# Kernel optimization log

Hardware: AMD Instinct MI355X
Metric: run time of the kernel (lower is better)

The kernel has to match this reference:

```python
import jax, jax.numpy as jnp
import numpy as np

B, S, D, H = 2, 2048, 1024, 16
HD = D // H  # head dim = 64


def setup_inputs() -> dict:
    key = jax.random.key(0)
    ks = jax.random.split(key, 8)
    s = 0.02
    return {
        "Q": jax.random.normal(ks[0], (B, S, D), jnp.float32),
        "K": jax.random.normal(ks[1], (B, S, D), jnp.float32),
        "V": jax.random.normal(ks[2], (B, S, D), jnp.float32),
        "mask": jax.random.randint(ks[3], (1, 1, S, S), 0, 2, jnp.int32),
        "Wq": jax.random.normal(ks[4], (D, D), jnp.float32) * s,
        "bq": jnp.zeros((D,), jnp.float32),
        "Wk": jax.random.normal(ks[5], (D, D), jnp.float32) * s,
        "bk": jnp.zeros((D,), jnp.float32),
        "Wv": jax.random.normal(ks[6], (D, D), jnp.float32) * s,
        "bv": jnp.zeros((D,), jnp.float32),
        "Wo": jax.random.normal(ks[7], (D, D), jnp.float32) * s,
        "bo": jnp.zeros((D,), jnp.float32),
    }


def reference(Q, K, V, mask, Wq, bq, Wk, bk, Wv, bv, Wo, bo):
    b = Q.shape[0]
    # QKV projections, split into heads: [B,S,D] -> [B,H,S,HD]
    q = (Q @ Wq + bq).reshape(b, -1, H, HD).transpose(0, 2, 1, 3)
    k = (K @ Wk + bk).reshape(b, -1, H, HD).transpose(0, 2, 1, 3)
    v = (V @ Wv + bv).reshape(b, -1, H, HD).transpose(0, 2, 1, 3)
    # scaled dot-product attention with full [B,H,S,S] scores (as in source)
    scale = jnp.sqrt(jnp.asarray(HD, q.dtype))
    scores = jnp.einsum("bhqd,bhkd->bhqk", q, k) / scale
    scores = jnp.where(mask == 0, -jnp.inf, scores)
    attn = jax.nn.softmax(scores, axis=-1)
    ctx = jnp.einsum("bhqk,bhkd->bhqd", attn, v)
    # merge heads and output projection
    concat = ctx.transpose(0, 2, 1, 3).reshape(b, -1, H * HD)
    return concat @ Wo + bo
```

## Files before the change

### kernel.cpp

```cpp
#include <hip/hip_runtime.h>


using s8v = __attribute__((ext_vector_type(8))) short;
using f4v = __attribute__((ext_vector_type(4))) float;
typedef unsigned long long u64;

__device__ __forceinline__ unsigned short f2bf(float f) {
  union { float f; unsigned int u; } v; v.f = f;
  return (unsigned short)((v.u + 0x7fffu + ((v.u >> 16) & 1u)) >> 16);
}

__device__ __forceinline__ void gll16(const void* g, void* l) {
  __builtin_amdgcn_global_load_lds(
      (const __attribute__((address_space(1))) unsigned int*)g,
      (__attribute__((address_space(3))) unsigned int*)l, 16, 0, 0);
}

__global__ void prep_kernel(const float* __restrict__ Q, const float* __restrict__ K,
                            const float* __restrict__ V,
                            unsigned short* __restrict__ qb, unsigned short* __restrict__ kb,
                            unsigned short* __restrict__ vb,
                            const float* __restrict__ W0, const float* __restrict__ W1,
                            const float* __restrict__ W2, const float* __restrict__ W3,
                            unsigned short* __restrict__ T0, unsigned short* __restrict__ T1,
                            unsigned short* __restrict__ T2, unsigned short* __restrict__ T3,
                            const int* __restrict__ mask, u64* __restrict__ bm) {
  __shared__ unsigned short t[64][72];
  const int bid = blockIdx.x, tid = threadIdx.x;
  if (bid < 12288) {
    int z = bid >> 12;
    int idx = (bid & 4095) * 256 + tid;
    const float* in = (z == 0) ? Q : (z == 1) ? K : V;
    unsigned short* out = (z == 0) ? qb : (z == 1) ? kb : vb;
    float4 v = ((const float4*)in)[idx];
    ushort4 o;
    o.x = f2bf(v.x); o.y = f2bf(v.y); o.z = f2bf(v.z); o.w = f2bf(v.w);
    ((ushort4*)out)[idx] = o;
  } else if (bid < 13312) {
    int b = bid - 12288;
    int z = b >> 8, rem = b & 255;
    int k0 = (rem >> 4) * 64, n0 = (rem & 15) * 64;
    const float* W = (z == 0) ? W0 : (z == 1) ? W1 : (z == 2) ? W2 : W3;
    unsigned short* Wt = (z == 0) ? T0 : (z == 1) ? T1 : (z == 2) ? T2 : T3;
    for (int p = 0; p < 4; ++p) {
      int idx = p * 256 + tid;
      int row = idx >> 4, c4 = idx & 15;
      float4 v = *(const float4*)&W[(size_t)(k0 + row) * 1024 + n0 + c4 * 4];
      t[row][c4 * 4 + 0] = f2bf(v.x);
      t[row][c4 * 4 + 1] = f2bf(v.y);
      t[row][c4 * 4 + 2] = f2bf(v.z);
      t[row][c4 * 4 + 3] = f2bf(v.w);
    }
    __syncthreads();
    for (int p = 0; p < 2; ++p) {
      int idx = p * 256 + tid;
      int j = idx >> 3, c8 = idx & 7;
      unsigned short tmp[8];
      for (int i = 0; i < 8; ++i) tmp[i] = t[c8 * 8 + i][j];
      uint4 o;
      o.x = tmp[0] | ((unsigned)tmp[1] << 16);
      o.y = tmp[2] | ((unsigned)tmp[3] << 16);
      o.z = tmp[4] | ((unsigned)tmp[5] << 16);
      o.w = tmp[6] | ((unsigned)tmp[7] << 16);
      *(uint4*)&Wt[(size_t)(n0 + j) * 1024 + k0 + c8 * 8] = o;
    }
  } else {
    int b = bid - 13312;
    int gw = (b * 256 + tid) >> 6;
    int lane = tid & 63;
    int mv = mask[(size_t)gw * 64 + lane];
    u64 bal = __ballot(mv != 0);
    if (lane == 0) bm[gw] = bal;
  }
}

__global__ __launch_bounds__(256) void proj3_kernel(
    const unsigned short* __restrict__ A0, const unsigned short* __restrict__ A1,
    const unsigned short* __restrict__ A2,
    const unsigned short* __restrict__ W0, const unsigned short* __restrict__ W1,
    const unsigned short* __restrict__ W2,
    const float* __restrict__ b0, const float* __restrict__ b1, const float* __restrict__ b2,
    unsigned short* __restrict__ oq, unsigned short* __restrict__ ok,
    unsigned short* __restrict__ ovt) {
  const int z = blockIdx.z;
  const unsigned short* A  = (z == 0) ? A0 : (z == 1) ? A1 : A2;
  const unsigned short* Wt = (z == 0) ? W0 : (z == 1) ? W1 : W2;
  const float* bias        = (z == 0) ? b0 : (z == 1) ? b1 : b2;

  __shared__ __align__(16) unsigned short As[64 * 32];
  __shared__ __align__(16) unsigned short Bs[128 * 32];

  const int tid = threadIdx.x;
  const int lane = tid & 63, w = tid >> 6, ln = lane & 15, quad = lane >> 4;
  const int wm = (w & 1) * 32, wn = (w >> 1) * 64;
  const int m0 = blockIdx.x * 64, n0 = blockIdx.y * 128;

  const int slr = lane >> 2;
  const int schunk = (lane & 3) ^ ((lane >> 3) & 3);
  const int cfrag = (quad ^ ((ln >> 1) & 3)) * 8;

  f4v zero = {0.f, 0.f, 0.f, 0.f};
  f4v acc[2][4];
  for (int mi = 0; mi < 2; ++mi)
    for (int ni = 0; ni < 4; ++ni) acc[mi][ni] = zero;

  for (int kt = 0; kt < 1024; kt += 32) {
    __syncthreads();
    gll16(&A[(size_t)(m0 + w * 16 + slr) * 1024 + kt + schunk * 8],        &As[(w * 16) * 32]);
    gll16(&Wt[(size_t)(n0 + w * 32 + slr) * 1024 + kt + schunk * 8],       &Bs[(w * 32) * 32]);
    gll16(&Wt[(size_t)(n0 + w * 32 + 16 + slr) * 1024 + kt + schunk * 8],  &Bs[(w * 32 + 16) * 32]);
    __syncthreads();
    s8v a[2], b[4];
    for (int mi = 0; mi < 2; ++mi) a[mi] = *(const s8v*)&As[(wm + mi * 16 + ln) * 32 + cfrag];
    for (int ni = 0; ni < 4; ++ni) b[ni] = *(const s8v*)&Bs[(wn + ni * 16 + ln) * 32 + cfrag];
    if (z < 2) {
      for (int mi = 0; mi < 2; ++mi)
        for (int ni = 0; ni < 4; ++ni)
          acc[mi][ni] = __builtin_amdgcn_mfma_f32_16x16x32_bf16(a[mi], b[ni], acc[mi][ni], 0, 0, 0);
    } else {
      for (int mi = 0; mi < 2; ++mi)
        for (int ni = 0; ni < 4; ++ni)
          acc[mi][ni] = __builtin_amdgcn_mfma_f32_16x16x32_bf16(b[ni], a[mi], acc[mi][ni], 0, 0, 0);
    }
  }

  if (z < 2) {
    const float qscale = (z == 0) ? 0.18033688f : 1.0f;
    unsigned short* outp = (z == 0) ? oq : ok;
    for (int mi = 0; mi < 2; ++mi) {
      int rb = m0 + wm + mi * 16 + quad * 4;
      int b_ = rb >> 11;
      for (int ni = 0; ni < 4; ++ni) {
        int col = n0 + wn + ni * 16 + ln;
        float bvv = bias[col];
        int h = col >> 6, hd = col & 63;
        size_t ob = (size_t)(b_ * 16 + h) * 2048;
        for (int r = 0; r < 4; ++r) {
          int s = (rb + r) & 2047;
          outp[(ob + s) * 64 + hd] = f2bf((acc[mi][ni][r] + bvv) * qscale);
        }
      }
    }
  } else {
    for (int ni = 0; ni < 4; ++ni) {
      for (int r = 0; r < 4; ++r) {
        int colw = n0 + wn + ni * 16 + quad * 4 + r;
        int h = colw >> 6, hd = colw & 63;
        float bvv = bias[colw];
        for (int mi = 0; mi < 2; ++mi) {
          int sg = m0 + wm + mi * 16 + ln;
          int b_ = sg >> 11, ss = sg & 2047;
          ovt[((size_t)(b_ * 16 + h) * 64 + hd) * 2048 + ss] = f2bf(acc[mi][ni][r] + bvv);
        }
      }
    }
  }
}

__global__ __launch_bounds__(512) void flash_kernel(
    const unsigned short* __restrict__ q, const unsigned short* __restrict__ k,
    const unsigned short* __restrict__ vt, const u64* __restrict__ bm,
    unsigned short* __restrict__ ctx) {
  __shared__ __align__(16) unsigned short qp_s[128][72];
  __shared__ __align__(16) unsigned short k_s[64][72];
  __shared__ __align__(16) unsigned short v_s[80][72];

  const int tid = threadIdx.x;
  const int lane = tid & 63, w = tid >> 6, ln = lane & 15, quad = lane >> 4;
  const int q0 = blockIdx.x * 128;
  const int bh = blockIdx.y;
  const unsigned short* qg  = q  + ((size_t)bh * 2048 + q0) * 64;
  const unsigned short* kgb = k  + (size_t)bh * 2048 * 64;
  const unsigned short* vgb = vt + (size_t)bh * 64 * 2048;

  for (int j = 0; j < 3; ++j) {
    int idx = j * 512 + tid;
    if (idx < 16 * 72) ((unsigned short*)v_s[64])[idx] = 0;
  }
  for (int p = 0; p < 2; ++p) {
    int c = p * 512 + tid;
    int row = c >> 3, c8 = c & 7;
    *(uint4*)&qp_s[row][c8 * 8] = *(const uint4*)&qg[(size_t)row * 64 + c8 * 8];
  }
  __syncthreads();
  if (tid < 64) v_s[64][tid] = 0x3F80;
  __syncthreads();

  s8v aq0 = *(const s8v*)&qp_s[w * 16 + ln][quad * 8];
  s8v aq1 = *(const s8v*)&qp_s[w * 16 + ln][32 + quad * 8];
  s8v bones0 = *(const s8v*)&v_s[64 + ln][quad * 8];
  s8v bones1 = *(const s8v*)&v_s[64 + ln][32 + quad * 8];

  const int srow = tid >> 3, sc8 = tid & 7;

  const u64* bmr = bm + (size_t)(q0 + w * 16 + ln) * 32;

  uint4 kr = *(const uint4*)&kgb[(size_t)srow * 64 + sc8 * 8];
  uint4 vr = *(const uint4*)&vgb[(size_t)srow * 2048 + sc8 * 8];
  u64 mwc = bmr[0], mwn;

  f4v zero = {0.f, 0.f, 0.f, 0.f};
  f4v l_acc = zero;
  f4v o_acc[4];
  for (int ni = 0; ni < 4; ++ni) o_acc[ni] = zero;

  for (int kt = 0; kt < 2048; kt += 64) {
    *(uint4*)&k_s[srow][sc8 * 8] = kr;
    *(uint4*)&v_s[srow][sc8 * 8] = vr;
    if (kt + 64 < 2048) {
      int ktn = kt + 64;
      kr = *(const uint4*)&kgb[(size_t)(ktn + srow) * 64 + sc8 * 8];
      vr = *(const uint4*)&vgb[(size_t)srow * 2048 + ktn + sc8 * 8];
      mwn = bmr[ktn >> 6];
    }
    __syncthreads();

    f4v sc[4];
    for (int ni = 0; ni < 4; ++ni) {
      s8v ak0 = *(const s8v*)&k_s[ni * 16 + ln][quad * 8];
      s8v ak1 = *(const s8v*)&k_s[ni * 16 + ln][32 + quad * 8];
      f4v t = zero;
      t = __builtin_amdgcn_mfma_f32_16x16x32_bf16(ak0, aq0, t, 0, 0, 0);
      t = __builtin_amdgcn_mfma_f32_16x16x32_bf16(ak1, aq1, t, 0, 0, 0);
      sc[ni] = t;
    }

    {
      u64 m = mwc >> (quad * 4);
      unsigned mlo = (unsigned)m, mhi = (unsigned)(m >> 32);
      for (int ni = 0; ni < 4; ++ni) {
        unsigned msel = ((ni < 2) ? mlo : mhi) >> ((ni & 1) * 16);
        unsigned u0 = __float_as_uint(__builtin_amdgcn_exp2f(sc[ni][0]) * (float)(msel & 1u));
        unsigned u1 = __float_as_uint(__builtin_amdgcn_exp2f(sc[ni][1]) * (float)((msel >> 1) & 1u));
        unsigned u2 = __float_as_uint(__builtin_amdgcn_exp2f(sc[ni][2]) * (float)((msel >> 2) & 1u));
        unsigned u3 = __float_as_uint(__builtin_amdgcn_exp2f(sc[ni][3]) * (float)((msel >> 3) & 1u));
        unsigned plo = __builtin_amdgcn_perm(u1, u0, 0x07060302);
        unsigned phi = __builtin_amdgcn_perm(u3, u2, 0x07060302);
        *(u64*)&qp_s[w * 16 + ln][ni * 16 + quad * 4] = plo | ((u64)phi << 32);
      }
      mwc = mwn;
    }

    s8v ap0 = *(const s8v*)&qp_s[w * 16 + ln][quad * 8];
    s8v ap1 = *(const s8v*)&qp_s[w * 16 + ln][32 + quad * 8];
    for (int ni = 0; ni < 4; ++ni) {
      s8v bv0 = *(const s8v*)&v_s[ni * 16 + ln][quad * 8];
      s8v bv1 = *(const s8v*)&v_s[ni * 16 + ln][32 + quad * 8];
      o_acc[ni] = __builtin_amdgcn_mfma_f32_16x16x32_bf16(ap0, bv0, o_acc[ni], 0, 0, 0);
      o_acc[ni] = __builtin_amdgcn_mfma_f32_16x16x32_bf16(ap1, bv1, o_acc[ni], 0, 0, 0);
    }
    l_acc = __builtin_amdgcn_mfma_f32_16x16x32_bf16(ap0, bones0, l_acc, 0, 0, 0);
    l_acc = __builtin_amdgcn_mfma_f32_16x16x32_bf16(ap1, bones1, l_acc, 0, 0, 0);
    __syncthreads();
  }

  int b_ = bh >> 4, h = bh & 15;
  for (int r = 0; r < 4; ++r) {
    float lr = __shfl(l_acc[r], quad * 16);
    float inv = 1.f / lr;
    int srow_ = q0 + w * 16 + quad * 4 + r;
    size_t base = ((size_t)b_ * 2048 + srow_) * 1024 + h * 64;
    for (int ni = 0; ni < 4; ++ni)
      ctx[base + ni * 16 + ln] = f2bf(o_acc[ni][r] * inv);
  }
}

__global__ __launch_bounds__(256) void gemm_out_kernel(
    const unsigned short* __restrict__ A, const unsigned short* __restrict__ Wt,
    const float* __restrict__ bias, float* __restrict__ out) {
  __shared__ __align__(16) unsigned short As[64 * 32];
  __shared__ __align__(16) unsigned short Bs[128 * 32];

  const int tid = threadIdx.x;
  const int lane = tid & 63, w = tid >> 6, ln = lane & 15, quad = lane >> 4;
  const int wm = (w & 1) * 32, wn = (w >> 1) * 64;
  const int m0 = blockIdx.x * 64, n0 = blockIdx.y * 128;

  const int slr = lane >> 2;
  const int schunk = (lane & 3) ^ ((lane >> 3) & 3);
  const int cfrag = (quad ^ ((ln >> 1) & 3)) * 8;

  f4v zero = {0.f, 0.f, 0.f, 0.f};
  f4v acc[2][4];
  for (int mi = 0; mi < 2; ++mi)
    for (int ni = 0; ni < 4; ++ni) acc[mi][ni] = zero;

  for (int kt = 0; kt < 1024; kt += 32) {
    __syncthreads();
    gll16(&A[(size_t)(m0 + w * 16 + slr) * 1024 + kt + schunk * 8],        &As[(w * 16) * 32]);
    gll16(&Wt[(size_t)(n0 + w * 32 + slr) * 1024 + kt + schunk * 8],       &Bs[(w * 32) * 32]);
    gll16(&Wt[(size_t)(n0 + w * 32 + 16 + slr) * 1024 + kt + schunk * 8],  &Bs[(w * 32 + 16) * 32]);
    __syncthreads();
    s8v a[2], b[4];
    for (int mi = 0; mi < 2; ++mi) a[mi] = *(const s8v*)&As[(wm + mi * 16 + ln) * 32 + cfrag];
    for (int ni = 0; ni < 4; ++ni) b[ni] = *(const s8v*)&Bs[(wn + ni * 16 + ln) * 32 + cfrag];
    for (int mi = 0; mi < 2; ++mi)
      for (int ni = 0; ni < 4; ++ni)
        acc[mi][ni] = __builtin_amdgcn_mfma_f32_16x16x32_bf16(a[mi], b[ni], acc[mi][ni], 0, 0, 0);
  }

  for (int mi = 0; mi < 2; ++mi) {
    int rb = m0 + wm + mi * 16 + quad * 4;
    for (int ni = 0; ni < 4; ++ni) {
      int col = n0 + wn + ni * 16 + ln;
      float bvv = bias[col];
      for (int r = 0; r < 4; ++r)
        out[(size_t)(rb + r) * 1024 + col] = acc[mi][ni][r] + bvv;
    }
  }
}

extern "C" void kernel_launch(void* const* d_in, const int* in_sizes, int n_in,
                              void* d_out, int out_size, void* d_ws, size_t ws_size,
                              hipStream_t stream) {
  const float* Q  = (const float*)d_in[0];
  const float* K  = (const float*)d_in[1];
  const float* V  = (const float*)d_in[2];
  const int* mask = (const int*)d_in[3];
  const float* Wq = (const float*)d_in[4];
  const float* bq = (const float*)d_in[5];
  const float* Wk = (const float*)d_in[6];
  const float* bk = (const float*)d_in[7];
  const float* Wv = (const float*)d_in[8];
  const float* bv = (const float*)d_in[9];
  const float* Wo = (const float*)d_in[10];
  const float* bo = (const float*)d_in[11];
  float* out = (float*)d_out;

  char* ws = (char*)d_ws;
  const size_t MB = 1u << 20;
  unsigned short* qb  = (unsigned short*)(ws + 0 * MB);
  unsigned short* kb  = (unsigned short*)(ws + 8 * MB);
  unsigned short* vb  = (unsigned short*)(ws + 16 * MB);
  unsigned short* wqt = (unsigned short*)(ws + 24 * MB);
  unsigned short* wkt = (unsigned short*)(ws + 26 * MB);
  unsigned short* wvt = (unsigned short*)(ws + 28 * MB);
  unsigned short* wot = (unsigned short*)(ws + 30 * MB);
  unsigned short* qh  = (unsigned short*)(ws + 32 * MB);
  unsigned short* kh  = (unsigned short*)(ws + 40 * MB);
  unsigned short* vth = (unsigned short*)(ws + 48 * MB);
  u64* bm             = (u64*)(ws + 56 * MB);
  unsigned short* ctx = (unsigned short*)(ws + 16 * MB);

  prep_kernel<<<29696, 256, 0, stream>>>(Q, K, V, qb, kb, vb,
                                         Wq, Wk, Wv, Wo, wqt, wkt, wvt, wot,
                                         mask, bm);
  proj3_kernel<<<dim3(64, 8, 3), 256, 0, stream>>>(qb, kb, vb, wqt, wkt, wvt,
                                                   bq, bk, bv, qh, kh, vth);
  flash_kernel<<<dim3(16, 32), 512, 0, stream>>>(qh, kh, vth, bm, ctx);
  gemm_out_kernel<<<dim3(64, 8), 256, 0, stream>>>(ctx, wot, bo, out);
}
```

Measured before the change: 258.0 us.

## Rework flash attention on 32x32 MFMA with register-resident P and double-buffered K/V

The attention kernel drops from 8 waves of 16 query rows to 4 waves of 32 rows and uses 32x32x16 bf16 MFMAs. The P tile is repacked into A-operand layout in registers with v_permlane32_swap instead of being written to and read back from LDS. K/V tiles are double-buffered in LDS so the next tile is staged during compute, leaving one barrier per iteration. Each wave now holds more accumulators, so register pressure rises and occupancy may fall.

```diff
diff --git a/kernel.cpp b/kernel.cpp
--- a/kernel.cpp
+++ b/kernel.cpp
@@ -3,11 +3,16 @@
 
 using s8v = __attribute__((ext_vector_type(8))) short;
 using f4v = __attribute__((ext_vector_type(4))) float;
+using f16v = __attribute__((ext_vector_type(16))) float;
 typedef unsigned long long u64;
 
 __device__ __forceinline__ unsigned short f2bf(float f) {
   union { float f; unsigned int u; } v; v.f = f;
   return (unsigned short)((v.u + 0x7fffu + ((v.u >> 16) & 1u)) >> 16);
+}
+
+__device__ __forceinline__ unsigned pkbf(float lo, float hi2) {
+  return __builtin_amdgcn_perm(__float_as_uint(hi2), __float_as_uint(lo), 0x07060302);
 }
 
 __device__ __forceinline__ void gll16(const void* g, void* l) {
@@ -157,111 +162,137 @@
   }
 }
 
-__global__ __launch_bounds__(512) void flash_kernel(
+__global__ __launch_bounds__(256) void flash_kernel(
     const unsigned short* __restrict__ q, const unsigned short* __restrict__ k,
     const unsigned short* __restrict__ vt, const u64* __restrict__ bm,
     unsigned short* __restrict__ ctx) {
-  __shared__ __align__(16) unsigned short qp_s[128][72];
-  __shared__ __align__(16) unsigned short k_s[64][72];
-  __shared__ __align__(16) unsigned short v_s[80][72];
+  __shared__ __align__(16) unsigned short k_s[2][64][72];
+  __shared__ __align__(16) unsigned short v_s[2][64][72];
 
   const int tid = threadIdx.x;
-  const int lane = tid & 63, w = tid >> 6, ln = lane & 15, quad = lane >> 4;
+  const int lane = tid & 63, w = tid >> 6;
+  const int l31 = lane & 31, hi = lane >> 5;
   const int q0 = blockIdx.x * 128;
   const int bh = blockIdx.y;
   const unsigned short* qg  = q  + ((size_t)bh * 2048 + q0) * 64;
   const unsigned short* kgb = k  + (size_t)bh * 2048 * 64;
   const unsigned short* vgb = vt + (size_t)bh * 64 * 2048;
 
-  for (int j = 0; j < 3; ++j) {
-    int idx = j * 512 + tid;
-    if (idx < 16 * 72) ((unsigned short*)v_s[64])[idx] = 0;
-  }
-  for (int p = 0; p < 2; ++p) {
-    int c = p * 512 + tid;
-    int row = c >> 3, c8 = c & 7;
-    *(uint4*)&qp_s[row][c8 * 8] = *(const uint4*)&qg[(size_t)row * 64 + c8 * 8];
-  }
+  const int qrow = w * 32 + l31;
+  s8v qf[4];
+#pragma unroll
+  for (int c = 0; c < 4; ++c)
+    qf[c] = *(const s8v*)&qg[(size_t)qrow * 64 + c * 16 + hi * 8];
+
+  const u64* bmr = bm + (size_t)(q0 + qrow) * 32;
+
+  s8v ones;
+#pragma unroll
+  for (int i = 0; i < 8; ++i) ones[i] = (short)0x3F80;
+
+  const int srow = tid >> 3, sc8 = tid & 7;
+
+  uint4 kr0 = *(const uint4*)&kgb[(size_t)srow * 64 + sc8 * 8];
+  uint4 kr1 = *(const uint4*)&kgb[(size_t)(srow + 32) * 64 + sc8 * 8];
+  uint4 vr0 = *(const uint4*)&vgb[(size_t)srow * 2048 + sc8 * 8];
+  uint4 vr1 = *(const uint4*)&vgb[(size_t)(srow + 32) * 2048 + sc8 * 8];
+  *(uint4*)&k_s[0][srow][sc8 * 8] = kr0;
+  *(uint4*)&k_s[0][srow + 32][sc8 * 8] = kr1;
+  *(uint4*)&v_s[0][srow][sc8 * 8] = vr0;
+  *(uint4*)&v_s[0][srow + 32][sc8 * 8] = vr1;
+  kr0 = *(const uint4*)&kgb[(size_t)(64 + srow) * 64 + sc8 * 8];
+  kr1 = *(const uint4*)&kgb[(size_t)(64 + srow + 32) * 64 + sc8 * 8];
+  vr0 = *(const uint4*)&vgb[(size_t)srow * 2048 + 64 + sc8 * 8];
+  vr1 = *(const uint4*)&vgb[(size_t)(srow + 32) * 2048 + 64 + sc8 * 8];
   __syncthreads();
-  if (tid < 64) v_s[64][tid] = 0x3F80;
-  __syncthreads();
-
-  s8v aq0 = *(const s8v*)&qp_s[w * 16 + ln][quad * 8];
-  s8v aq1 = *(const s8v*)&qp_s[w * 16 + ln][32 + quad * 8];
-  s8v bones0 = *(const s8v*)&v_s[64 + ln][quad * 8];
-  s8v bones1 = *(const s8v*)&v_s[64 + ln][32 + quad * 8];
-
-  const int srow = tid >> 3, sc8 = tid & 7;
-
-  const u64* bmr = bm + (size_t)(q0 + w * 16 + ln) * 32;
-
-  uint4 kr = *(const uint4*)&kgb[(size_t)srow * 64 + sc8 * 8];
-  uint4 vr = *(const uint4*)&vgb[(size_t)srow * 2048 + sc8 * 8];
-  u64 mwc = bmr[0], mwn;
-
-  f4v zero = {0.f, 0.f, 0.f, 0.f};
-  f4v l_acc = zero;
-  f4v o_acc[4];
-  for (int ni = 0; ni < 4; ++ni) o_acc[ni] = zero;
+
+  f16v o0, o1, lac;
+#pragma unroll
+  for (int i = 0; i < 16; ++i) { o0[i] = 0.f; o1[i] = 0.f; lac[i] = 0.f; }
 
   for (int kt = 0; kt < 2048; kt += 64) {
-    *(uint4*)&k_s[srow][sc8 * 8] = kr;
-    *(uint4*)&v_s[srow][sc8 * 8] = vr;
+    const int cur = (kt >> 6) & 1;
+    u64 mwc = bmr[kt >> 6];
+
     if (kt + 64 < 2048) {
-      int ktn = kt + 64;
-      kr = *(const uint4*)&kgb[(size_t)(ktn + srow) * 64 + sc8 * 8];
-      vr = *(const uint4*)&vgb[(size_t)srow * 2048 + ktn + sc8 * 8];
-      mwn = bmr[ktn >> 6];
-    }
-    __syncthreads();
-
-    f4v sc[4];
-    for (int ni = 0; ni < 4; ++ni) {
-      s8v ak0 = *(const s8v*)&k_s[ni * 16 + ln][quad * 8];
-      s8v ak1 = *(const s8v*)&k_s[ni * 16 + ln][32 + quad * 8];
-      f4v t = zero;
-      t = __builtin_amdgcn_mfma_f32_16x16x32_bf16(ak0, aq0, t, 0, 0, 0);
-      t = __builtin_amdgcn_mfma_f32_16x16x32_bf16(ak1, aq1, t, 0, 0, 0);
-      sc[ni] = t;
-    }
-
-    {
-      u64 m = mwc >> (quad * 4);
-      unsigned mlo = (unsigned)m, mhi = (unsigned)(m >> 32);
-      for (int ni = 0; ni < 4; ++ni) {
-        unsigned msel = ((ni < 2) ? mlo : mhi) >> ((ni & 1) * 16);
-        unsigned u0 = __float_as_uint(__builtin_amdgcn_exp2f(sc[ni][0]) * (float)(msel & 1u));
-        unsigned u1 = __float_as_uint(__builtin_amdgcn_exp2f(sc[ni][1]) * (float)((msel >> 1) & 1u));
-        unsigned u2 = __float_as_uint(__builtin_amdgcn_exp2f(sc[ni][2]) * (float)((msel >> 2) & 1u));
-        unsigned u3 = __float_as_uint(__builtin_amdgcn_exp2f(sc[ni][3]) * (float)((msel >> 3) & 1u));
-        unsigned plo = __builtin_amdgcn_perm(u1, u0, 0x07060302);
-        unsigned phi = __builtin_amdgcn_perm(u3, u2, 0x07060302);
-        *(u64*)&qp_s[w * 16 + ln][ni * 16 + quad * 4] = plo | ((u64)phi << 32);
-      }
-      mwc = mwn;
-    }
-
-    s8v ap0 = *(const s8v*)&qp_s[w * 16 + ln][quad * 8];
-    s8v ap1 = *(const s8v*)&qp_s[w * 16 + ln][32 + quad * 8];
-    for (int ni = 0; ni < 4; ++ni) {
-      s8v bv0 = *(const s8v*)&v_s[ni * 16 + ln][quad * 8];
-      s8v bv1 = *(const s8v*)&v_s[ni * 16 + ln][32 + quad * 8];
-      o_acc[ni] = __builtin_amdgcn_mfma_f32_16x16x32_bf16(ap0, bv0, o_acc[ni], 0, 0, 0);
-      o_acc[ni] = __builtin_amdgcn_mfma_f32_16x16x32_bf16(ap1, bv1, o_acc[ni], 0, 0, 0);
-    }
-    l_acc = __builtin_amdgcn_mfma_f32_16x16x32_bf16(ap0, bones0, l_acc, 0, 0, 0);
-    l_acc = __builtin_amdgcn_mfma_f32_16x16x32_bf16(ap1, bones1, l_acc, 0, 0, 0);
-    __syncthreads();
-  }
-
-  int b_ = bh >> 4, h = bh & 15;
-  for (int r = 0; r < 4; ++r) {
-    float lr = __shfl(l_acc[r], quad * 16);
-    float inv = 1.f / lr;
-    int srow_ = q0 + w * 16 + quad * 4 + r;
-    size_t base = ((size_t)b_ * 2048 + srow_) * 1024 + h * 64;
-    for (int ni = 0; ni < 4; ++ni)
-      ctx[base + ni * 16 + ln] = f2bf(o_acc[ni][r] * inv);
+      const int nxt = cur ^ 1;
+      *(uint4*)&k_s[nxt][srow][sc8 * 8] = kr0;
+      *(uint4*)&k_s[nxt][srow + 32][sc8 * 8] = kr1;
+      *(uint4*)&v_s[nxt][srow][sc8 * 8] = vr0;
+      *(uint4*)&v_s[nxt][srow + 32][sc8 * 8] = vr1;
+      if (kt + 128 < 2048) {
+        const int kn = kt + 128;
+        kr0 = *(const uint4*)&kgb[(size_t)(kn + srow) * 64 + sc8 * 8];
+        kr1 = *(const uint4*)&kgb[(size_t)(kn + srow + 32) * 64 + sc8 * 8];
+        vr0 = *(const uint4*)&vgb[(size_t)srow * 2048 + kn + sc8 * 8];
+        vr1 = *(const uint4*)&vgb[(size_t)(srow + 32) * 2048 + kn + sc8 * 8];
+      }
+    }
+
+    f16v s0, s1;
+#pragma unroll
+    for (int i = 0; i < 16; ++i) { s0[i] = 0.f; s1[i] = 0.f; }
+#pragma unroll
+    for (int c = 0; c < 4; ++c) {
+      s8v ak0 = *(const s8v*)&k_s[cur][l31][c * 16 + hi * 8];
+      s8v ak1 = *(const s8v*)&k_s[cur][32 + l31][c * 16 + hi * 8];
+      s0 = __builtin_amdgcn_mfma_f32_32x32x16_bf16(ak0, qf[c], s0, 0, 0, 0);
+      s1 = __builtin_amdgcn_mfma_f32_32x32x16_bf16(ak1, qf[c], s1, 0, 0, 0);
+    }
+
+    const u64 mq = mwc >> (4 * hi);
+    s8v pf[4];
+#pragma unroll
+    for (int ni = 0; ni < 2; ++ni) {
+      const unsigned half = (unsigned)(mq >> (32 * ni));
+      float p[16];
+#pragma unroll
+      for (int g = 0; g < 4; ++g) {
+        const unsigned nib = (half >> (8 * g)) & 0xFu;
+#pragma unroll
+        for (int m = 0; m < 4; ++m) {
+          const float sv = (ni ? s1[g * 4 + m] : s0[g * 4 + m]);
+          p[g * 4 + m] = __builtin_amdgcn_exp2f(sv) * (float)((nib >> m) & 1u);
+        }
+      }
+#pragma unroll
+      for (int kcl = 0; kcl < 2; ++kcl) {
+        const int rb = 8 * kcl;
+        unsigned x0 = pkbf(p[rb + 0], p[rb + 1]);
+        unsigned x1 = pkbf(p[rb + 2], p[rb + 3]);
+        unsigned y0 = pkbf(p[rb + 4], p[rb + 5]);
+        unsigned y1 = pkbf(p[rb + 6], p[rb + 7]);
+        asm("v_permlane32_swap_b32 %0, %1" : "+v"(x0), "+v"(y0));
+        asm("v_permlane32_swap_b32 %0, %1" : "+v"(x1), "+v"(y1));
+        union { uint4 u; s8v v; } cv;
+        cv.u = make_uint4(x0, x1, y0, y1);
+        pf[ni * 2 + kcl] = cv.v;
+      }
+    }
+
+#pragma unroll
+    for (int kc = 0; kc < 4; ++kc)
+      lac = __builtin_amdgcn_mfma_f32_32x32x16_bf16(pf[kc], ones, lac, 0, 0, 0);
+
+#pragma unroll
+    for (int kc = 0; kc < 4; ++kc) {
+      s8v bv0 = *(const s8v*)&v_s[cur][l31][kc * 16 + hi * 8];
+      s8v bv1 = *(const s8v*)&v_s[cur][32 + l31][kc * 16 + hi * 8];
+      o0 = __builtin_amdgcn_mfma_f32_32x32x16_bf16(pf[kc], bv0, o0, 0, 0, 0);
+      o1 = __builtin_amdgcn_mfma_f32_32x32x16_bf16(pf[kc], bv1, o1, 0, 0, 0);
+    }
+    __syncthreads();
+  }
+
+  const int b_ = bh >> 4, h = bh & 15;
+#pragma unroll
+  for (int r = 0; r < 16; ++r) {
+    const int ql = (r & 3) + 8 * (r >> 2) + 4 * hi;
+    const float inv = 1.f / lac[r];
+    const int srw = q0 + w * 32 + ql;
+    const size_t base = ((size_t)b_ * 2048 + srw) * 1024 + h * 64;
+    ctx[base + l31] = f2bf(o0[r] * inv);
+    ctx[base + 32 + l31] = f2bf(o1[r] * inv);
   }
 }
 
@@ -347,6 +378,6 @@
                                          mask, bm);
   proj3_kernel<<<dim3(64, 8, 3), 256, 0, stream>>>(qb, kb, vb, wqt, wkt, wvt,
                                                    bq, bk, bv, qh, kh, vth);
-  flash_kernel<<<dim3(16, 32), 512, 0, stream>>>(qh, kh, vth, bm, ctx);
+  flash_kernel<<<dim3(16, 32), 256, 0, stream>>>(qh, kh, vth, bm, ctx);
   gemm_out_kernel<<<dim3(64, 8), 256, 0, stream>>>(ctx, wot, bo, out);
 }
```

After: 264.0 us. 2.3% more time.
